# Optimization experiments

Hardware: AMD Instinct MI355X
Metric: run time of the kernel (lower is better)

Reference implementation:

```python
import jax, jax.numpy as jnp
import numpy as np

N_NODES = 100000
N_EDGES = 1600000
D_IN, D_H, D_OUT = 128, 64, 32


def _linear_init(key, out_dim, in_dim):
    # torch.nn.Linear default init: U(-1/sqrt(in), 1/sqrt(in))
    bound = 1.0 / np.sqrt(in_dim)
    return jax.random.uniform(key, (out_dim, in_dim), jnp.float32, -bound, bound)


def setup_inputs() -> dict:
    key = jax.random.key(0)
    ks = jax.random.split(key, 8)
    x = jax.random.normal(ks[0], (N_NODES, D_IN), dtype=jnp.float32)
    edge_index = jax.random.randint(ks[1], (2, N_EDGES), 0, N_NODES, dtype=jnp.int64)
    return {
        "x": x,
        "edge_index": edge_index,
        # SAGEConv layer 1: lin_l (neighbor agg, with bias), lin_r (root, no bias)
        "W1_l": _linear_init(ks[2], D_H, D_IN),
        "b1": jnp.zeros((D_H,), jnp.float32),
        "W1_r": _linear_init(ks[3], D_H, D_IN),
        # SAGEConv layer 2
        "W2_l": _linear_init(ks[4], D_OUT, D_H),
        "b2": jnp.zeros((D_OUT,), jnp.float32),
        "W2_r": _linear_init(ks[5], D_OUT, D_H),
    }


def _sage_conv(x, src, dst, W_l, b_l, W_r):
    """PyG SAGEConv with mean aggregation: lin_l(mean_{j in N(i)} x_j) + lin_r(x_i)."""
    n = x.shape[0]
    # scatter-mean of source features onto destination nodes
    agg = jax.ops.segment_sum(x[src], dst, num_segments=n)          # [N, d]
    deg = jax.ops.segment_sum(jnp.ones_like(dst, dtype=x.dtype), dst, num_segments=n)
    mean = agg / jnp.maximum(deg, 1.0)[:, None]
    return mean @ W_l.T + b_l + x @ W_r.T


def reference(x, edge_index, W1_l, b1, W1_r, W2_l, b2, W2_r):
    src, dst = edge_index[0], edge_index[1]
    h = _sage_conv(x, src, dst, W1_l, b1, W1_r)
    h = jax.nn.relu(h)
    # dropout p=0.5 is identity in eval mode
    return _sage_conv(h, src, dst, W2_l, b2, W2_r)
```

## Files before the change

### kernel.cpp

```cpp
#include <hip/hip_runtime.h>


namespace {
constexpr int N = 100000;
constexpr int E = 1600000;
constexpr int NT16 = N / 16;
constexpr int NCHUNK = 64;
constexpr int CHUNK_N = 1600;
constexpr int CAP = 28000;
constexpr int PA_BLOCKS = 256;
constexpr int PER_BLK = E / PA_BLOCKS;
}

using bf16x8 = __attribute__((ext_vector_type(8))) short;
using f32x4  = __attribute__((ext_vector_type(4))) float;

__device__ __forceinline__ unsigned short f2bf(float f) {
    unsigned u = __builtin_bit_cast(unsigned, f);
    u += 0x7FFFu + ((u >> 16) & 1u);
    return (unsigned short)(u >> 16);
}

__device__ __forceinline__ bf16x8 load_frag8(const float* __restrict__ p) {
    const float4* p4 = (const float4*)p;
    float4 f0 = p4[0], f1 = p4[1];
    bf16x8 r;
    r[0] = f2bf(f0.x); r[1] = f2bf(f0.y); r[2] = f2bf(f0.z); r[3] = f2bf(f0.w);
    r[4] = f2bf(f1.x); r[5] = f2bf(f1.y); r[6] = f2bf(f1.z); r[7] = f2bf(f1.w);
    return r;
}

__device__ __forceinline__ float pk_lo(unsigned u) {
    return __builtin_bit_cast(float, u << 16);
}
__device__ __forceinline__ float pk_hi(unsigned u) {
    return __builtin_bit_cast(float, u & 0xFFFF0000u);
}
__device__ __forceinline__ unsigned pk2(float a, float b) {
    return (unsigned)f2bf(a) | ((unsigned)f2bf(b) << 16);
}


__global__ __launch_bounds__(256) void detect_dtype(const int* __restrict__ raw,
                                                    int* __restrict__ flag,
                                                    int* __restrict__ bcur) {
    if (threadIdx.x < NCHUNK) bcur[threadIdx.x] = 0;
    int any = 0;
#pragma unroll
    for (int k = 0; k < 64; ++k) {
        int i = threadIdx.x + k * 256;
        any |= raw[2 * i + 1];
    }
    unsigned long long b = __ballot(any != 0);
    __shared__ int acc[4];
    int w = threadIdx.x >> 6;
    if ((threadIdx.x & 63) == 0) acc[w] = (b != 0ULL) ? 1 : 0;
    __syncthreads();
    if (threadIdx.x == 0) *flag = acc[0] | acc[1] | acc[2] | acc[3];
}

__global__ __launch_bounds__(256) void bucket_edges(
        const int* __restrict__ raw, const int* __restrict__ flag,
        int* __restrict__ bcur, int2* __restrict__ bucket) {
    __shared__ int cnt[NCHUNK];
    __shared__ int res[NCHUNK];
    if (threadIdx.x < NCHUNK) cnt[threadIdx.x] = 0;
    __syncthreads();
    const int is32 = *flag;
    const int e0 = blockIdx.x * PER_BLK;
    for (int i = threadIdx.x; i < PER_BLK; i += 256) {
        int e = e0 + i;
        int d = is32 ? raw[E + e] : raw[2 * ((long long)E + e)];
        atomicAdd(&cnt[d / CHUNK_N], 1);
    }
    __syncthreads();
    if (threadIdx.x < NCHUNK) {
        res[threadIdx.x] = atomicAdd(&bcur[threadIdx.x], cnt[threadIdx.x]);
        cnt[threadIdx.x] = 0;
    }
    __syncthreads();
    for (int i = threadIdx.x; i < PER_BLK; i += 256) {
        int e = e0 + i;
        int d, s;
        if (is32) { d = raw[E + e]; s = raw[e]; }
        else      { d = raw[2 * ((long long)E + e)]; s = raw[2 * (long long)e]; }
        int c = d / CHUNK_N;
        int pos = res[c] + atomicAdd(&cnt[c], 1);
        if (pos < CAP) bucket[(size_t)c * CAP + pos] = make_int2(s, d);
    }
}

__global__ __launch_bounds__(1024) void build_csr(
        const int* __restrict__ bcur, const int2* __restrict__ bucket,
        int* __restrict__ rowstart, int* __restrict__ csr) {
    __shared__ int sc[2048];
    __shared__ int st[2048];
    __shared__ int sbase;
    const int chunk = blockIdx.x;
    const int lo = chunk * CHUNK_N;
    const int t = threadIdx.x;
    sc[t] = 0; sc[t + 1024] = 0;
    if (t == 0) {
        int bsum = 0;
        for (int c = 0; c < chunk; ++c) bsum += bcur[c];
        sbase = bsum;
    }
    __syncthreads();
    int n = bcur[chunk]; if (n > CAP) n = CAP;
    const int2* b = bucket + (size_t)chunk * CAP;
    for (int i = t; i < n; i += 1024)
        atomicAdd(&sc[b[i].y - lo], 1);
    __syncthreads();
    const int cA = sc[t], cB = sc[t + 1024];
    int* src = sc; int* dst = st;
    for (int off = 1; off < 2048; off <<= 1) {
        int vA = src[t] + ((t >= off) ? src[t - off] : 0);
        int vB = src[t + 1024] + src[t + 1024 - off];
        dst[t] = vA; dst[t + 1024] = vB;
        __syncthreads();
        int* tmp = src; src = dst; dst = tmp;
    }
    const int base = sbase;
    const int exA = base + src[t] - cA;
    const int exB = base + src[t + 1024] - cB;
    const int lim = N - lo;
    if (t < lim) rowstart[lo + t] = exA;
    if (t + 1024 < CHUNK_N && t + 1024 < lim) rowstart[lo + t + 1024] = exB;
    if (chunk == 0 && t == 0) rowstart[N] = E;
    dst[t] = exA; dst[t + 1024] = exB;
    __syncthreads();
    for (int i = t; i < n; i += 1024) {
        int2 sd = b[i];
        int pos = atomicAdd(&dst[sd.y - lo], 1);
        csr[pos] = sd.x;
    }
}

__global__ __launch_bounds__(256) void transform1_mfma(
        const float* __restrict__ x, const float* __restrict__ W1l,
        const float* __restrict__ W1r, unsigned short* __restrict__ z1b,
        unsigned short* __restrict__ r1b) {
    const int lane = threadIdx.x & 63;
    const int gw = blockIdx.x * 4 + (threadIdx.x >> 6);
    const int q = gw & 1;
    const int r16 = lane & 15;
    const int kgrp = lane >> 4;

    bf16x8 wf[2][2][4];
#pragma unroll
    for (int m = 0; m < 2; ++m) {
        const float* W = m ? W1r : W1l;
#pragma unroll
        for (int c = 0; c < 2; ++c) {
            const float* pw = W + (size_t)(q * 32 + c * 16 + r16) * 128 + kgrp * 8;
#pragma unroll
            for (int kb = 0; kb < 4; ++kb)
                wf[m][c][kb] = load_frag8(pw + kb * 32);
        }
    }

    const int stride = (gridDim.x * 4) >> 1;
    for (int t = gw >> 1; t < NT16; t += stride) {
        const float* px = x + ((size_t)t * 16 + r16) * 128 + kgrp * 8;
        bf16x8 af[4];
#pragma unroll
        for (int kb = 0; kb < 4; ++kb) af[kb] = load_frag8(px + kb * 32);

        f32x4 a00 = {0.f,0.f,0.f,0.f}, a01 = {0.f,0.f,0.f,0.f};
        f32x4 a10 = {0.f,0.f,0.f,0.f}, a11 = {0.f,0.f,0.f,0.f};
#pragma unroll
        for (int kb = 0; kb < 4; ++kb) {
            a00 = __builtin_amdgcn_mfma_f32_16x16x32_bf16(af[kb], wf[0][0][kb], a00, 0, 0, 0);
            a01 = __builtin_amdgcn_mfma_f32_16x16x32_bf16(af[kb], wf[0][1][kb], a01, 0, 0, 0);
            a10 = __builtin_amdgcn_mfma_f32_16x16x32_bf16(af[kb], wf[1][0][kb], a10, 0, 0, 0);
            a11 = __builtin_amdgcn_mfma_f32_16x16x32_bf16(af[kb], wf[1][1][kb], a11, 0, 0, 0);
        }
#pragma unroll
        for (int i = 0; i < 4; ++i) {
            size_t row = (size_t)t * 16 + kgrp * 4 + i;
            z1b[row * 64 + q * 32 +  0 + r16] = f2bf(a00[i]);
            z1b[row * 64 + q * 32 + 16 + r16] = f2bf(a01[i]);
            r1b[row * 64 + q * 32 +  0 + r16] = f2bf(a10[i]);
            r1b[row * 64 + q * 32 + 16 + r16] = f2bf(a11[i]);
        }
    }
}

__global__ __launch_bounds__(256) void transform2_mfma(
        const unsigned short* __restrict__ hb, const float* __restrict__ W2l,
        const float* __restrict__ W2r, unsigned short* __restrict__ z2b,
        unsigned short* __restrict__ r2b) {
    const int lane = threadIdx.x & 63;
    const int gw = blockIdx.x * 4 + (threadIdx.x >> 6);
    const int r16 = lane & 15;
    const int kgrp = lane >> 4;

    bf16x8 wf[2][2][2];
#pragma unroll
    for (int m = 0; m < 2; ++m) {
        const float* W = m ? W2r : W2l;
#pragma unroll
        for (int c = 0; c < 2; ++c) {
            const float* pw = W + (size_t)(c * 16 + r16) * 64 + kgrp * 8;
#pragma unroll
            for (int kb = 0; kb < 2; ++kb)
                wf[m][c][kb] = load_frag8(pw + kb * 32);
        }
    }

    for (int t = gw; t < NT16; t += gridDim.x * 4) {
        const unsigned short* ph = hb + ((size_t)t * 16 + r16) * 64 + kgrp * 8;
        bf16x8 af[2];
        af[0] = *(const bf16x8*)(ph);
        af[1] = *(const bf16x8*)(ph + 32);

        f32x4 a00 = {0.f,0.f,0.f,0.f}, a01 = {0.f,0.f,0.f,0.f};
        f32x4 a10 = {0.f,0.f,0.f,0.f}, a11 = {0.f,0.f,0.f,0.f};
#pragma unroll
        for (int kb = 0; kb < 2; ++kb) {
            a00 = __builtin_amdgcn_mfma_f32_16x16x32_bf16(af[kb], wf[0][0][kb], a00, 0, 0, 0);
            a01 = __builtin_amdgcn_mfma_f32_16x16x32_bf16(af[kb], wf[0][1][kb], a01, 0, 0, 0);
            a10 = __builtin_amdgcn_mfma_f32_16x16x32_bf16(af[kb], wf[1][0][kb], a10, 0, 0, 0);
            a11 = __builtin_amdgcn_mfma_f32_16x16x32_bf16(af[kb], wf[1][1][kb], a11, 0, 0, 0);
        }
#pragma unroll
        for (int i = 0; i < 4; ++i) {
            size_t row = (size_t)t * 16 + kgrp * 4 + i;
            z2b[row * 32 +  0 + r16] = f2bf(a00[i]);
            z2b[row * 32 + 16 + r16] = f2bf(a01[i]);
            r2b[row * 32 +  0 + r16] = f2bf(a10[i]);
            r2b[row * 32 + 16 + r16] = f2bf(a11[i]);
        }
    }
}

__global__ __launch_bounds__(256) void agg1_fused(
        const int* __restrict__ rowstart, const int* __restrict__ csr,
        const uint2* __restrict__ z1d, const uint2* __restrict__ r1d,
        const float* __restrict__ b1, uint2* __restrict__ hb) {
    const int n = blockIdx.x * 4 + (threadIdx.x >> 6);
    if (n >= N) return;
    const int lane = threadIdx.x & 63;
    const int quad = lane >> 4;
    const int fl = lane & 15;
    const int beg = rowstart[n], end = rowstart[n + 1];
    float a0 = 0.f, a1 = 0.f, a2 = 0.f, a3 = 0.f;
    int p = beg;
    for (; p + 16 <= end; p += 16) {
        int c0 = csr[p + quad],      c1 = csr[p + 4 + quad];
        int c2 = csr[p + 8 + quad],  c3 = csr[p + 12 + quad];
        uint2 u0 = z1d[(size_t)c0 * 16 + fl];
        uint2 u1 = z1d[(size_t)c1 * 16 + fl];
        uint2 u2 = z1d[(size_t)c2 * 16 + fl];
        uint2 u3 = z1d[(size_t)c3 * 16 + fl];
        a0 += pk_lo(u0.x) + pk_lo(u1.x) + pk_lo(u2.x) + pk_lo(u3.x);
        a1 += pk_hi(u0.x) + pk_hi(u1.x) + pk_hi(u2.x) + pk_hi(u3.x);
        a2 += pk_lo(u0.y) + pk_lo(u1.y) + pk_lo(u2.y) + pk_lo(u3.y);
        a3 += pk_hi(u0.y) + pk_hi(u1.y) + pk_hi(u2.y) + pk_hi(u3.y);
    }
    for (; p + 4 <= end; p += 4) {
        int c = csr[p + quad];
        uint2 u = z1d[(size_t)c * 16 + fl];
        a0 += pk_lo(u.x); a1 += pk_hi(u.x);
        a2 += pk_lo(u.y); a3 += pk_hi(u.y);
    }
    if (p < end) {
        int rem = end - p;
        if (quad < rem) {
            int c = csr[p + quad];
            uint2 u = z1d[(size_t)c * 16 + fl];
            a0 += pk_lo(u.x); a1 += pk_hi(u.x);
            a2 += pk_lo(u.y); a3 += pk_hi(u.y);
        }
    }
    a0 += __shfl_xor(a0, 16, 64); a1 += __shfl_xor(a1, 16, 64);
    a2 += __shfl_xor(a2, 16, 64); a3 += __shfl_xor(a3, 16, 64);
    a0 += __shfl_xor(a0, 32, 64); a1 += __shfl_xor(a1, 32, 64);
    a2 += __shfl_xor(a2, 32, 64); a3 += __shfl_xor(a3, 32, 64);
    if (lane < 16) {
        float inv = (end > beg) ? 1.0f / (float)(end - beg) : 0.f;
        uint2 rr = r1d[(size_t)n * 16 + fl];
        float4 bv = ((const float4*)b1)[fl];
        float h0 = fmaxf(a0 * inv + bv.x + pk_lo(rr.x), 0.f);
        float h1 = fmaxf(a1 * inv + bv.y + pk_hi(rr.x), 0.f);
        float h2 = fmaxf(a2 * inv + bv.z + pk_lo(rr.y), 0.f);
        float h3 = fmaxf(a3 * inv + bv.w + pk_hi(rr.y), 0.f);
        uint2 o;
        o.x = pk2(h0, h1);
        o.y = pk2(h2, h3);
        hb[(size_t)n * 16 + fl] = o;
    }
}

__global__ __launch_bounds__(256) void agg2_fused(
        const int* __restrict__ rowstart, const int* __restrict__ csr,
        const uint2* __restrict__ z2d, const uint2* __restrict__ r2d,
        const float* __restrict__ b2, float* __restrict__ out) {
    const int n = blockIdx.x * 4 + (threadIdx.x >> 6);
    if (n >= N) return;
    const int lane = threadIdx.x & 63;
    const int oct = lane >> 3;
    const int fl = lane & 7;
    const int beg = rowstart[n], end = rowstart[n + 1];
    float a0 = 0.f, a1 = 0.f, a2 = 0.f, a3 = 0.f;
    int p = beg;
    for (; p + 8 <= end; p += 8) {
        int c = csr[p + oct];
        uint2 u = z2d[(size_t)c * 8 + fl];
        a0 += pk_lo(u.x); a1 += pk_hi(u.x);
        a2 += pk_lo(u.y); a3 += pk_hi(u.y);
    }
    if (p < end) {
        int rem = end - p;
        if (oct < rem) {
            int c = csr[p + oct];
            uint2 u = z2d[(size_t)c * 8 + fl];
            a0 += pk_lo(u.x); a1 += pk_hi(u.x);
            a2 += pk_lo(u.y); a3 += pk_hi(u.y);
        }
    }
    a0 += __shfl_xor(a0, 8, 64);  a1 += __shfl_xor(a1, 8, 64);
    a2 += __shfl_xor(a2, 8, 64);  a3 += __shfl_xor(a3, 8, 64);
    a0 += __shfl_xor(a0, 16, 64); a1 += __shfl_xor(a1, 16, 64);
    a2 += __shfl_xor(a2, 16, 64); a3 += __shfl_xor(a3, 16, 64);
    a0 += __shfl_xor(a0, 32, 64); a1 += __shfl_xor(a1, 32, 64);
    a2 += __shfl_xor(a2, 32, 64); a3 += __shfl_xor(a3, 32, 64);
    if (lane < 8) {
        float inv = (end > beg) ? 1.0f / (float)(end - beg) : 0.f;
        uint2 rr = r2d[(size_t)n * 8 + fl];
        float4 bv = ((const float4*)b2)[fl];
        float4 o;
        o.x = a0 * inv + bv.x + pk_lo(rr.x);
        o.y = a1 * inv + bv.y + pk_hi(rr.x);
        o.z = a2 * inv + bv.z + pk_lo(rr.y);
        o.w = a3 * inv + bv.w + pk_hi(rr.y);
        ((float4*)out)[(size_t)n * 8 + fl] = o;
    }
}


extern "C" void kernel_launch(void* const* d_in, const int* in_sizes, int n_in,
                              void* d_out, int out_size, void* d_ws, size_t ws_size,
                              hipStream_t stream) {
    const float* x    = (const float*)d_in[0];
    const int*   raw  = (const int*)d_in[1];
    const float* W1l  = (const float*)d_in[2];
    const float* b1   = (const float*)d_in[3];
    const float* W1r  = (const float*)d_in[4];
    const float* W2l  = (const float*)d_in[5];
    const float* b2   = (const float*)d_in[6];
    const float* W2r  = (const float*)d_in[7];
    float* out = (float*)d_out;

    char* wsb = (char*)d_ws;
    unsigned short* z1b = (unsigned short*)wsb;
    unsigned short* z2b = (unsigned short*)wsb;
    unsigned short* r1b = (unsigned short*)(wsb + 16 * 1024 * 1024);
    unsigned short* r2b = (unsigned short*)(wsb + 16 * 1024 * 1024);
    unsigned short* hb  = (unsigned short*)(wsb + 48 * 1024 * 1024);
    int2* bucket = (int2*)(wsb + 64 * 1024 * 1024);

    int* ibase    = (int*)(wsb + 80 * 1024 * 1024);
    int* rowstart = ibase;
    int* csr      = ibase + N + 1;
    int* flag     = csr + E;
    int* bcur     = flag + 1;

    detect_dtype<<<1, 256, 0, stream>>>(raw, flag, bcur);
    bucket_edges<<<PA_BLOCKS, 256, 0, stream>>>(raw, flag, bcur, bucket);
    build_csr<<<NCHUNK, 1024, 0, stream>>>(bcur, bucket, rowstart, csr);

    transform1_mfma<<<1024, 256, 0, stream>>>(x, W1l, W1r, z1b, r1b);
    agg1_fused<<<(N + 3) / 4, 256, 0, stream>>>(rowstart, csr, (const uint2*)z1b,
                                                (const uint2*)r1b, b1, (uint2*)hb);

    transform2_mfma<<<1024, 256, 0, stream>>>(hb, W2l, W2r, z2b, r2b);
    agg2_fused<<<(N + 3) / 4, 256, 0, stream>>>(rowstart, csr, (const uint2*)z2b,
                                                (const uint2*)r2b, b2, out);
}
```

Before: 200.3 us.

## Merge edge bucketing and layer-1 transform into one launch; inline dtype detection

Combines the edge-bucketing kernel and the layer-1 MFMA feature transform into a single grid. The first blocks bucket edges while the remaining blocks compute x@W, so the two independent stages overlap instead of running back-to-back. The separate dtype-detection kernel is removed: each bucketing block checks its own slice of the edge array for int32 vs int64 layout, and bcur is zeroed with a memset. This cuts launch count and serialization. The per-block detection samples only 256 high words, so it could misjudge the dtype on unusual inputs.

```diff
diff --git a/kernel.cpp b/kernel.cpp
--- a/kernel.cpp
+++ b/kernel.cpp
@@ -10,6 +10,7 @@
 constexpr int CAP = 28000;
 constexpr int PA_BLOCKS = 256;
 constexpr int PER_BLK = E / PA_BLOCKS;
+constexpr int T1_BLOCKS = 1024;
 }
 
 using bf16x8 = __attribute__((ext_vector_type(8))) short;
@@ -40,53 +41,93 @@
     return (unsigned)f2bf(a) | ((unsigned)f2bf(b) << 16);
 }
 
-
-__global__ __launch_bounds__(256) void detect_dtype(const int* __restrict__ raw,
-                                                    int* __restrict__ flag,
-                                                    int* __restrict__ bcur) {
-    if (threadIdx.x < NCHUNK) bcur[threadIdx.x] = 0;
-    int any = 0;
-#pragma unroll
-    for (int k = 0; k < 64; ++k) {
-        int i = threadIdx.x + k * 256;
-        any |= raw[2 * i + 1];
-    }
-    unsigned long long b = __ballot(any != 0);
-    __shared__ int acc[4];
-    int w = threadIdx.x >> 6;
-    if ((threadIdx.x & 63) == 0) acc[w] = (b != 0ULL) ? 1 : 0;
-    __syncthreads();
-    if (threadIdx.x == 0) *flag = acc[0] | acc[1] | acc[2] | acc[3];
-}
-
-__global__ __launch_bounds__(256) void bucket_edges(
-        const int* __restrict__ raw, const int* __restrict__ flag,
-        int* __restrict__ bcur, int2* __restrict__ bucket) {
+__global__ __launch_bounds__(256) void bucket_t1(
+        const int* __restrict__ raw, int* __restrict__ bcur,
+        int2* __restrict__ bucket,
+        const float* __restrict__ x, const float* __restrict__ W1l,
+        const float* __restrict__ W1r, unsigned short* __restrict__ z1b,
+        unsigned short* __restrict__ r1b) {
     __shared__ int cnt[NCHUNK];
     __shared__ int res[NCHUNK];
-    if (threadIdx.x < NCHUNK) cnt[threadIdx.x] = 0;
-    __syncthreads();
-    const int is32 = *flag;
-    const int e0 = blockIdx.x * PER_BLK;
-    for (int i = threadIdx.x; i < PER_BLK; i += 256) {
-        int e = e0 + i;
-        int d = is32 ? raw[E + e] : raw[2 * ((long long)E + e)];
-        atomicAdd(&cnt[d / CHUNK_N], 1);
-    }
-    __syncthreads();
-    if (threadIdx.x < NCHUNK) {
-        res[threadIdx.x] = atomicAdd(&bcur[threadIdx.x], cnt[threadIdx.x]);
-        cnt[threadIdx.x] = 0;
-    }
-    __syncthreads();
-    for (int i = threadIdx.x; i < PER_BLK; i += 256) {
-        int e = e0 + i;
-        int d, s;
-        if (is32) { d = raw[E + e]; s = raw[e]; }
-        else      { d = raw[2 * ((long long)E + e)]; s = raw[2 * (long long)e]; }
-        int c = d / CHUNK_N;
-        int pos = res[c] + atomicAdd(&cnt[c], 1);
-        if (pos < CAP) bucket[(size_t)c * CAP + pos] = make_int2(s, d);
+    __shared__ int sdet[4];
+
+    if (blockIdx.x < PA_BLOCKS) {
+        const int e0 = blockIdx.x * PER_BLK;
+        int any = raw[2 * (e0 + threadIdx.x) + 1];
+        unsigned long long bl = __ballot(any != 0);
+        int w = threadIdx.x >> 6;
+        if ((threadIdx.x & 63) == 0) sdet[w] = (bl != 0ULL) ? 1 : 0;
+        if (threadIdx.x < NCHUNK) cnt[threadIdx.x] = 0;
+        __syncthreads();
+        const int is32 = sdet[0] | sdet[1] | sdet[2] | sdet[3];
+
+        for (int i = threadIdx.x; i < PER_BLK; i += 256) {
+            int e = e0 + i;
+            int d = is32 ? raw[E + e] : raw[2 * ((long long)E + e)];
+            atomicAdd(&cnt[d / CHUNK_N], 1);
+        }
+        __syncthreads();
+        if (threadIdx.x < NCHUNK) {
+            res[threadIdx.x] = atomicAdd(&bcur[threadIdx.x], cnt[threadIdx.x]);
+            cnt[threadIdx.x] = 0;
+        }
+        __syncthreads();
+        for (int i = threadIdx.x; i < PER_BLK; i += 256) {
+            int e = e0 + i;
+            int d, s;
+            if (is32) { d = raw[E + e]; s = raw[e]; }
+            else      { d = raw[2 * ((long long)E + e)]; s = raw[2 * (long long)e]; }
+            int c = d / CHUNK_N;
+            int pos = res[c] + atomicAdd(&cnt[c], 1);
+            if (pos < CAP) bucket[(size_t)c * CAP + pos] = make_int2(s, d);
+        }
+        return;
+    }
+
+    const int bid = blockIdx.x - PA_BLOCKS;
+    const int lane = threadIdx.x & 63;
+    const int gw = bid * 4 + (threadIdx.x >> 6);
+    const int q = gw & 1;
+    const int r16 = lane & 15;
+    const int kgrp = lane >> 4;
+
+    bf16x8 wf[2][2][4];
+#pragma unroll
+    for (int m = 0; m < 2; ++m) {
+        const float* W = m ? W1r : W1l;
+#pragma unroll
+        for (int c = 0; c < 2; ++c) {
+            const float* pw = W + (size_t)(q * 32 + c * 16 + r16) * 128 + kgrp * 8;
+#pragma unroll
+            for (int kb = 0; kb < 4; ++kb)
+                wf[m][c][kb] = load_frag8(pw + kb * 32);
+        }
+    }
+
+    const int stride = (T1_BLOCKS * 4) >> 1;
+    for (int t = gw >> 1; t < NT16; t += stride) {
+        const float* px = x + ((size_t)t * 16 + r16) * 128 + kgrp * 8;
+        bf16x8 af[4];
+#pragma unroll
+        for (int kb = 0; kb < 4; ++kb) af[kb] = load_frag8(px + kb * 32);
+
+        f32x4 a00 = {0.f,0.f,0.f,0.f}, a01 = {0.f,0.f,0.f,0.f};
+        f32x4 a10 = {0.f,0.f,0.f,0.f}, a11 = {0.f,0.f,0.f,0.f};
+#pragma unroll
+        for (int kb = 0; kb < 4; ++kb) {
+            a00 = __builtin_amdgcn_mfma_f32_16x16x32_bf16(af[kb], wf[0][0][kb], a00, 0, 0, 0);
+            a01 = __builtin_amdgcn_mfma_f32_16x16x32_bf16(af[kb], wf[0][1][kb], a01, 0, 0, 0);
+            a10 = __builtin_amdgcn_mfma_f32_16x16x32_bf16(af[kb], wf[1][0][kb], a10, 0, 0, 0);
+            a11 = __builtin_amdgcn_mfma_f32_16x16x32_bf16(af[kb], wf[1][1][kb], a11, 0, 0, 0);
+        }
+#pragma unroll
+        for (int i = 0; i < 4; ++i) {
+            size_t row = (size_t)t * 16 + kgrp * 4 + i;
+            z1b[row * 64 + q * 32 +  0 + r16] = f2bf(a00[i]);
+            z1b[row * 64 + q * 32 + 16 + r16] = f2bf(a01[i]);
+            r1b[row * 64 + q * 32 +  0 + r16] = f2bf(a10[i]);
+            r1b[row * 64 + q * 32 + 16 + r16] = f2bf(a11[i]);
+        }
     }
 }
 
@@ -133,56 +174,6 @@
         int2 sd = b[i];
         int pos = atomicAdd(&dst[sd.y - lo], 1);
         csr[pos] = sd.x;
-    }
-}
-
-__global__ __launch_bounds__(256) void transform1_mfma(
-        const float* __restrict__ x, const float* __restrict__ W1l,
-        const float* __restrict__ W1r, unsigned short* __restrict__ z1b,
-        unsigned short* __restrict__ r1b) {
-    const int lane = threadIdx.x & 63;
-    const int gw = blockIdx.x * 4 + (threadIdx.x >> 6);
-    const int q = gw & 1;
-    const int r16 = lane & 15;
-    const int kgrp = lane >> 4;
-
-    bf16x8 wf[2][2][4];
-#pragma unroll
-    for (int m = 0; m < 2; ++m) {
-        const float* W = m ? W1r : W1l;
-#pragma unroll
-        for (int c = 0; c < 2; ++c) {
-            const float* pw = W + (size_t)(q * 32 + c * 16 + r16) * 128 + kgrp * 8;
-#pragma unroll
-            for (int kb = 0; kb < 4; ++kb)
-                wf[m][c][kb] = load_frag8(pw + kb * 32);
-        }
-    }
-
-    const int stride = (gridDim.x * 4) >> 1;
-    for (int t = gw >> 1; t < NT16; t += stride) {
-        const float* px = x + ((size_t)t * 16 + r16) * 128 + kgrp * 8;
-        bf16x8 af[4];
-#pragma unroll
-        for (int kb = 0; kb < 4; ++kb) af[kb] = load_frag8(px + kb * 32);
-
-        f32x4 a00 = {0.f,0.f,0.f,0.f}, a01 = {0.f,0.f,0.f,0.f};
-        f32x4 a10 = {0.f,0.f,0.f,0.f}, a11 = {0.f,0.f,0.f,0.f};
-#pragma unroll
-        for (int kb = 0; kb < 4; ++kb) {
-            a00 = __builtin_amdgcn_mfma_f32_16x16x32_bf16(af[kb], wf[0][0][kb], a00, 0, 0, 0);
-            a01 = __builtin_amdgcn_mfma_f32_16x16x32_bf16(af[kb], wf[0][1][kb], a01, 0, 0, 0);
-            a10 = __builtin_amdgcn_mfma_f32_16x16x32_bf16(af[kb], wf[1][0][kb], a10, 0, 0, 0);
-            a11 = __builtin_amdgcn_mfma_f32_16x16x32_bf16(af[kb], wf[1][1][kb], a11, 0, 0, 0);
-        }
-#pragma unroll
-        for (int i = 0; i < 4; ++i) {
-            size_t row = (size_t)t * 16 + kgrp * 4 + i;
-            z1b[row * 64 + q * 32 +  0 + r16] = f2bf(a00[i]);
-            z1b[row * 64 + q * 32 + 16 + r16] = f2bf(a01[i]);
-            r1b[row * 64 + q * 32 +  0 + r16] = f2bf(a10[i]);
-            r1b[row * 64 + q * 32 + 16 + r16] = f2bf(a11[i]);
-        }
     }
 }
 
@@ -363,14 +354,13 @@
     int* ibase    = (int*)(wsb + 80 * 1024 * 1024);
     int* rowstart = ibase;
     int* csr      = ibase + N + 1;
-    int* flag     = csr + E;
-    int* bcur     = flag + 1;
-
-    detect_dtype<<<1, 256, 0, stream>>>(raw, flag, bcur);
-    bucket_edges<<<PA_BLOCKS, 256, 0, stream>>>(raw, flag, bcur, bucket);
+    int* bcur     = csr + E;
+
+    hipMemsetAsync(bcur, 0, NCHUNK * sizeof(int), stream);
+    bucket_t1<<<PA_BLOCKS + T1_BLOCKS, 256, 0, stream>>>(
+        raw, bcur, bucket, x, W1l, W1r, z1b, r1b);
     build_csr<<<NCHUNK, 1024, 0, stream>>>(bcur, bucket, rowstart, csr);
 
-    transform1_mfma<<<1024, 256, 0, stream>>>(x, W1l, W1r, z1b, r1b);
     agg1_fused<<<(N + 3) / 4, 256, 0, stream>>>(rowstart, csr, (const uint2*)z1b,
                                                 (const uint2*)r1b, b1, (uint2*)hb);
 
```

Result: faster. 193.2 us (-3.6%).
